# Performance work log

Hardware: AMD Instinct MI355X
Metric: run time of the kernel (lower is better)

The kernel has to match this reference:

```python
import jax, jax.numpy as jnp
import numpy as np
import math

HEAD_DIM = 64           # d_model // n_heads // 2
N_HEADS = 8
LAMBDA_INIT = 0.8 - 0.6 * math.exp(-0.3 * 6)  # depth=6
EPS = 1e-5


def setup_inputs() -> dict:
    key = jax.random.key(0)
    ks = jax.random.split(key, 8)
    B, T, S = 2, 2048, 2048
    return {
        "queries": jax.random.normal(ks[0], (B, 2 * N_HEADS, T, HEAD_DIM), jnp.float32),
        "keys": jax.random.normal(ks[1], (B, 2 * N_HEADS, S, HEAD_DIM), jnp.float32),
        "values": jax.random.normal(ks[2], (B, N_HEADS, S, 2 * HEAD_DIM), jnp.float32),
        "lambda_q1": 0.02 * jax.random.normal(ks[3], (HEAD_DIM,), jnp.float32),
        "lambda_k1": 0.02 * jax.random.normal(ks[4], (HEAD_DIM,), jnp.float32),
        "lambda_q2": 0.02 * jax.random.normal(ks[5], (HEAD_DIM,), jnp.float32),
        "lambda_k2": 0.02 * jax.random.normal(ks[6], (HEAD_DIM,), jnp.float32),
        "subln_weight": jnp.ones((2 * HEAD_DIM,), jnp.float32),
        "tgt_len": 2048,
        "src_len": 2048,
        "attn_mask": jnp.zeros((1,), jnp.bool_),
    }


def reference(queries, keys, values, lambda_q1, lambda_k1, lambda_q2, lambda_k2,
              subln_weight, tgt_len, src_len, attn_mask):
    B = queries.shape[0]
    scaling = HEAD_DIM ** -0.5
    q = queries * scaling
    # [B, 2H, T, S]
    attn_w = jnp.einsum('bhtd,bhsd->bhts', q, keys)
    attn_w = jax.nn.softmax(attn_w.astype(jnp.float32), axis=-1).astype(queries.dtype)
    lam1 = jnp.exp(jnp.sum(lambda_q1 * lambda_k1))
    lam2 = jnp.exp(jnp.sum(lambda_q2 * lambda_k2))
    lam_full = lam1 - lam2 + LAMBDA_INIT
    attn_w = attn_w.reshape(B, N_HEADS, 2, tgt_len, src_len)
    attn_w = attn_w[:, :, 0] - lam_full * attn_w[:, :, 1]   # [B, H, T, S]
    attn = jnp.einsum('bhts,bhse->bhte', attn_w, values)    # [B, H, T, 2*HEAD_DIM]
    # RMSNorm over last dim
    normed = attn * jax.lax.rsqrt(jnp.mean(jnp.square(attn.astype(jnp.float32)), axis=-1, keepdims=True) + EPS).astype(attn.dtype)
    normed = normed * subln_weight
    out = normed * (1.0 - LAMBDA_INIT)
    out = out.transpose(0, 2, 1, 3).reshape(B, tgt_len, N_HEADS * 2 * HEAD_DIM)
    return out
```

## Files before the change

### kernel.cpp

```cpp
#include <hip/hip_runtime.h>
#include <math.h>


#define NT    2048
#define D     64
#define DV    128
#define TQ    64
#define TS    32
#define NROUND (NT / (2 * TS))

#define LAMBDA_INIT 0.70082066706704814f
#define OUT_SCALE   0.29917933293295186f
#define QSCALE      0.18033688011112042f

typedef __attribute__((ext_vector_type(8)))  short    short8;
typedef __attribute__((ext_vector_type(4)))  short    short4v;
typedef __attribute__((ext_vector_type(8)))  _Float16 half8;
typedef __attribute__((ext_vector_type(2)))  __fp16   fp16x2;
typedef __attribute__((ext_vector_type(4)))  float    f32x4;
typedef unsigned short u16;
typedef unsigned int   u32;

#define MFMAH(a, b, c)  __builtin_amdgcn_mfma_f32_16x16x32_f16(a, b, c, 0, 0, 0)
#define MFMA16(a, b, c) __builtin_amdgcn_mfma_f32_16x16x32_bf16(a, b, c, 0, 0, 0)

#if __has_builtin(__builtin_amdgcn_exp2f)
#define EXP2F(x) __builtin_amdgcn_exp2f(x)
#else
#define EXP2F(x) exp2f(x)
#endif

union Hu { half8 v; _Float16 e[8]; u16 s[8]; short8 sv; };

__device__ __forceinline__ u16 f2h(float x) {
    Hu u; u.e[0] = (_Float16)x; return u.s[0];
}

__global__ __launch_bounds__(256) void prep_kv(
    const float* __restrict__ Kg, const float* __restrict__ Vg,
    const float* __restrict__ lq1, const float* __restrict__ lk1,
    const float* __restrict__ lq2, const float* __restrict__ lk2,
    u16* __restrict__ Kf, u16* __restrict__ Vf, float* __restrict__ lamw)
{
    __shared__ u16 th[64 * 136];
    const int bid = blockIdx.x;
    const int t   = threadIdx.x;
    if (bid < 2048) {
        const int idx = (bid * 256 + t) * 8;
        const float4 a = *(const float4*)(Kg + idx);
        const float4 b = *(const float4*)(Kg + idx + 4);
        Hu H;
        H.e[0] = (_Float16)a.x; H.e[1] = (_Float16)a.y;
        H.e[2] = (_Float16)a.z; H.e[3] = (_Float16)a.w;
        H.e[4] = (_Float16)b.x; H.e[5] = (_Float16)b.y;
        H.e[6] = (_Float16)b.z; H.e[7] = (_Float16)b.w;
        *(short8*)(Kf + idx) = H.sv;
        return;
    }
    if (bid == 2048) {
        if (t == 0) {
            float t1 = 0.f, t2 = 0.f;
            for (int i = 0; i < D; ++i) {
                t1 = fmaf(lq1[i], lk1[i], t1);
                t2 = fmaf(lq2[i], lk2[i], t2);
            }
            lamw[0] = __expf(t1) - __expf(t2) + LAMBDA_INIT;
        }
        return;
    }
    const int i  = bid - 2049;
    const int bh = i >> 5;
    const int eb = (i >> 4) & 1;
    const int sb = i & 15;
    const size_t vbase = (size_t)bh * NT * DV + (size_t)sb * 128 * DV + eb * 64;
    {
        const int r0 = t >> 4;
        const int c4 = (t & 15) * 4;
        #pragma unroll
        for (int rr = 0; rr < 8; ++rr) {
            const int row = r0 + rr * 16;
            const float4 x = *(const float4*)(Vg + vbase + (size_t)row * DV + c4);
            th[(c4 + 0) * 136 + row] = f2h(x.x);
            th[(c4 + 1) * 136 + row] = f2h(x.y);
            th[(c4 + 2) * 136 + row] = f2h(x.z);
            th[(c4 + 3) * 136 + row] = f2h(x.w);
        }
    }
    __syncthreads();
    const int e  = t >> 2;
    const int g  = t & 3;
    const size_t orow = ((size_t)bh * DV + eb * 64 + e) * NT + sb * 128;
    #pragma unroll
    for (int c = 0; c < 4; ++c) {
        Hu o;
        #pragma unroll
        for (int j = 0; j < 8; ++j)
            o.s[j] = th[e * 136 + g * 32 + 4 * c + (j & 3) + 16 * (j >> 2)];
        *(short8*)(Vf + orow + g * 32 + c * 8) = o.sv;
    }
}

struct SmemF {
    union {
        short8 c[4096];
        struct {
            float epi[2][32][132];
            float lbuf[2][2][2][32];
        } e;
    };
};

__global__ __launch_bounds__(512, 4) void diffattn_mfma11(
    const float* __restrict__ Qg,
    const u16* __restrict__ Kf, const u16* __restrict__ Vf,
    const float* __restrict__ lamw,
    const float* __restrict__ Wg, float* __restrict__ Outg)
{
    __shared__ SmemF sm;

    const int tid    = threadIdx.x;
    const int wv     = tid >> 6;
    const int lane   = tid & 63;
    const int quad   = lane >> 4;
    const int lc     = lane & 15;
    const int stripe = wv & 1;
    const int hh     = (wv >> 1) & 1;
    const int ks     = wv >> 2;
    const int wig    = wv & 3;
    const int qt     = blockIdx.x;
    const int bh     = blockIdx.y;
    const int b      = bh >> 3, h = bh & 7;

    const int head2b = b * 16 + 2 * h;
    const int bh8    = b * 8 + h;
    const float lam  = lamw[0];

    half8 qf[2][2];
    {
        const size_t qhead = (size_t)(head2b + hh) * NT * D;
        #pragma unroll
        for (int nq = 0; nq < 2; ++nq) {
            const int row = qt * TQ + stripe * 32 + nq * 16 + lc;
            #pragma unroll
            for (int k0 = 0; k0 < 2; ++k0) {
                const int d0 = k0 * 32 + quad * 8;
                const float4 x = *(const float4*)(Qg + qhead + (size_t)row * D + d0);
                const float4 y = *(const float4*)(Qg + qhead + (size_t)row * D + d0 + 4);
                Hu q;
                q.e[0] = (_Float16)(x.x * QSCALE); q.e[1] = (_Float16)(x.y * QSCALE);
                q.e[2] = (_Float16)(x.z * QSCALE); q.e[3] = (_Float16)(x.w * QSCALE);
                q.e[4] = (_Float16)(y.x * QSCALE); q.e[5] = (_Float16)(y.y * QSCALE);
                q.e[6] = (_Float16)(y.z * QSCALE); q.e[7] = (_Float16)(y.w * QSCALE);
                qf[nq][k0] = q.v;
            }
        }
    }

    f32x4 O_[2][8];
    #pragma unroll
    for (int nq = 0; nq < 2; ++nq)
        #pragma unroll
        for (int nt = 0; nt < 8; ++nt) O_[nq][nt] = (f32x4){0.f, 0.f, 0.f, 0.f};
    float lac[2] = {0.f, 0.f};

    u32 gK[2], gV[2];
    int kDst[2], vDst[2];
    #pragma unroll
    for (int j = 0; j < 2; ++j) {
        const int ck  = wig * 128 + lane * 2 + j;
        const int hhs = ck >> 8;
        const int n   = (ck >> 3) & 31;
        const int db  = ck & 7;
        gK[j]   = (u32)(((head2b + hhs) * NT + n) * D + db * 8);
        kDst[j] = ks * 512 + hhs * 256 + n * 8 + (db ^ (n & 7));
        const int cv = wig * 128 + lane * 2 + j;
        const int e  = cv >> 2;
        const int u  = cv & 3;
        gV[j]   = (u32)((bh8 * DV + e) * NT + u * 8);
        vDst[j] = 1024 + ks * 512 + e * 4 + (u ^ ((e >> 1) & 3));
    }

    u32 kOff[2][2];
    #pragma unroll
    for (int k0 = 0; k0 < 2; ++k0)
        #pragma unroll
        for (int mt = 0; mt < 2; ++mt)
            kOff[k0][mt] = (u32)((ks * 512 + hh * 256 + (mt * 16 + lc) * 8 +
                                  ((4 * k0 + quad) ^ (lc & 7))) * 8);
    u32 vOff[8];
    {
        const int swzv = quad ^ ((lc >> 1) & 3);
        #pragma unroll
        for (int nt = 0; nt < 8; ++nt)
            vOff[nt] = (u32)((1024 + ks * 512 + (nt * 16 + lc) * 4 + swzv) * 8);
    }

    const u16* ldsu = (const u16*)&sm.c[0];

    short8 pk[2], pv[2];
    #pragma unroll
    for (int j = 0; j < 2; ++j) {
        pk[j] = *(const short8*)(Kf + gK[j] + (u32)ks * (TS * D));
        pv[j] = *(const short8*)(Vf + gV[j] + (u32)ks * TS);
    }
    sm.c[kDst[0]] = pk[0];
    sm.c[kDst[1]] = pk[1];
    sm.c[vDst[0]] = pv[0];
    sm.c[vDst[1]] = pv[1];
    {
        const u32 tn = (u32)(2 + ks);
        #pragma unroll
        for (int j = 0; j < 2; ++j) {
            pk[j] = *(const short8*)(Kf + gK[j] + tn * (TS * D));
            pv[j] = *(const short8*)(Vf + gV[j] + tn * TS);
        }
    }
    __syncthreads();

    const fp16x2 ones = {(__fp16)1.f, (__fp16)1.f};

    for (int r = 0; r < NROUND; ++r) {
        const u32 bo = ((u32)(r & 1)) << 14;

        f32x4 sf[2][2];
        #pragma unroll
        for (int mt = 0; mt < 2; ++mt)
            #pragma unroll
            for (int nq = 0; nq < 2; ++nq) sf[mt][nq] = (f32x4){0.f, 0.f, 0.f, 0.f};
        #pragma unroll
        for (int k0 = 0; k0 < 2; ++k0) {
            #pragma unroll
            for (int mt = 0; mt < 2; ++mt) {
                const half8 kfr = *(const half8*)(ldsu + bo + kOff[k0][mt]);
                #pragma unroll
                for (int nq = 0; nq < 2; ++nq)
                    sf[mt][nq] = MFMAH(kfr, qf[nq][k0], sf[mt][nq]);
            }
        }

        if (r < NROUND - 1) {
            const int cd = ((r & 1) ^ 1) << 11;
            sm.c[cd + kDst[0]] = pk[0];
            sm.c[cd + kDst[1]] = pk[1];
            sm.c[cd + vDst[0]] = pv[0];
            sm.c[cd + vDst[1]] = pv[1];
        }
        if (r < NROUND - 2) {
            const u32 tn = (u32)(2 * (r + 2) + ks);
            #pragma unroll
            for (int j = 0; j < 2; ++j) {
                pk[j] = *(const short8*)(Kf + gK[j] + tn * (TS * D));
                pv[j] = *(const short8*)(Vf + gV[j] + tn * TS);
            }
        }

        half8 a8[2];
        #pragma unroll
        for (int nq = 0; nq < 2; ++nq) {
            union { half8 v; fp16x2 h[4]; } a;
            float ls = lac[nq];
            #pragma unroll
            for (int mt = 0; mt < 2; ++mt)
                #pragma unroll
                for (int ip = 0; ip < 2; ++ip) {
                    const float p0 = EXP2F(sf[mt][nq][2 * ip]);
                    const float p1 = EXP2F(sf[mt][nq][2 * ip + 1]);
                    const fp16x2 h2 = __builtin_amdgcn_cvt_pkrtz(p0, p1);
                    a.h[mt * 2 + ip] = h2;
                    ls = __builtin_amdgcn_fdot2(h2, ones, ls, false);
                }
            lac[nq] = ls;
            a8[nq] = a.v;
        }

        #pragma unroll
        for (int nt = 0; nt < 8; ++nt) {
            const half8 vfr = *(const half8*)(ldsu + bo + vOff[nt]);
            #pragma unroll
            for (int nq = 0; nq < 2; ++nq)
                O_[nq][nt] = MFMAH(a8[nq], vfr, O_[nq][nt]);
        }

        __syncthreads();
    }

    {
        float s0 = lac[0], s1 = lac[1];
        s0 += __shfl_xor(s0, 16); s0 += __shfl_xor(s0, 32);
        s1 += __shfl_xor(s1, 16); s1 += __shfl_xor(s1, 32);
        if (quad == 0) {
            sm.e.lbuf[hh][ks][stripe][lc]      = s0;
            sm.e.lbuf[hh][ks][stripe][16 + lc] = s1;
        }
    }
    __syncthreads();
    float coef[2][4];
    #pragma unroll
    for (int nq = 0; nq < 2; ++nq)
        #pragma unroll
        for (int i = 0; i < 4; ++i) {
            const int row = nq * 16 + quad * 4 + i;
            const float lt = sm.e.lbuf[hh][0][stripe][row] +
                             sm.e.lbuf[hh][1][stripe][row];
            coef[nq][i] = (hh == 0) ? (1.f / lt) : (-lam / lt);
        }
    __syncthreads();
    const int pid = hh * 2 + ks;
    #pragma unroll
    for (int p = 0; p < 4; ++p) {
        if (pid == p) {
            #pragma unroll
            for (int nq = 0; nq < 2; ++nq)
                #pragma unroll
                for (int i = 0; i < 4; ++i) {
                    const int row = nq * 16 + quad * 4 + i;
                    #pragma unroll
                    for (int nt = 0; nt < 8; ++nt) {
                        const int col = nt * 16 + lc;
                        const float v = O_[nq][nt][i] * coef[nq][i];
                        if (p == 0) sm.e.epi[stripe][row][col] = v;
                        else        sm.e.epi[stripe][row][col] += v;
                    }
                }
        }
        __syncthreads();
    }
    {
        const int r0 = wv * 8 + (lane >> 3);
        const int st = r0 >> 5, ri = r0 & 31;
        const int e0 = (lane & 7) * 16;
        float x[16];
        float ssq = 0.f;
        #pragma unroll
        for (int m = 0; m < 16; m += 4) {
            const float4 t4 = *(const float4*)&sm.e.epi[st][ri][e0 + m];
            x[m] = t4.x; x[m + 1] = t4.y; x[m + 2] = t4.z; x[m + 3] = t4.w;
            ssq += t4.x * t4.x + t4.y * t4.y + t4.z * t4.z + t4.w * t4.w;
        }
        ssq += __shfl_xor(ssq, 1);
        ssq += __shfl_xor(ssq, 2);
        ssq += __shfl_xor(ssq, 4);
        const float rsq = rsqrtf(ssq * (1.f / 128.f) + 1e-5f) * OUT_SCALE;
        const int rowg = qt * TQ + r0;
        const size_t base =
            ((size_t)b * NT + rowg) * (size_t)(8 * DV) + (size_t)h * DV;
        #pragma unroll
        for (int m = 0; m < 16; m += 4) {
            const float4 w4 = *(const float4*)(Wg + e0 + m);
            float4 o4;
            o4.x = x[m] * rsq * w4.x;
            o4.y = x[m + 1] * rsq * w4.y;
            o4.z = x[m + 2] * rsq * w4.z;
            o4.w = x[m + 3] * rsq * w4.w;
            *(float4*)(Outg + base + e0 + m) = o4;
        }
    }
}

__device__ __forceinline__ unsigned short f2bf(float x) {
    unsigned u = __float_as_uint(x);
    return (unsigned short)((u + 0x7fffu + ((u >> 16) & 1u)) >> 16);
}
__device__ __forceinline__ float bf2f(unsigned short h) {
    return __uint_as_float(((unsigned)h) << 16);
}

struct SmemB {
    union {
        struct {
            short8 kh[2][264];
            short8 kl[2][264];
            short8 vh[516];
            short8 vl[516];
            unsigned short ph[2][2560];
            unsigned short pl[2][2560];
        } L;
        float epi[2][32][132];
    };
};

__global__ __launch_bounds__(256, 2) void diffattn_fb(
    const float* __restrict__ Qg, const float* __restrict__ Kg,
    const float* __restrict__ Vg,
    const float* __restrict__ lq1, const float* __restrict__ lk1,
    const float* __restrict__ lq2, const float* __restrict__ lk2,
    const float* __restrict__ Wg, float* __restrict__ Outg)
{
    __shared__ SmemB sm;
    const int tid = threadIdx.x;
    const int wv = tid >> 6, lane = tid & 63;
    const int quad = lane >> 4, lc = lane & 15;
    const int stripe = wv & 1, hh = wv >> 1;
    const int qt = blockIdx.x, bh = blockIdx.y;
    const int b = bh >> 3, h = bh & 7;
    const size_t koff0 = ((size_t)(b * 16 + 2 * h)) * NT * D;
    const size_t voff  = ((size_t)(b * 8 + h)) * NT * DV;
    float t1 = 0.f, t2 = 0.f;
    for (int i = 0; i < D; ++i) {
        t1 = fmaf(lq1[i], lk1[i], t1);
        t2 = fmaf(lq2[i], lk2[i], t2);
    }
    const float lam = __expf(t1) - __expf(t2) + LAMBDA_INIT;
    short8 qfh[2][2], qfl[2][2];
    {
        const size_t qhead = ((size_t)(b * 16 + 2 * h + hh)) * NT * D;
        #pragma unroll
        for (int mt = 0; mt < 2; ++mt)
            #pragma unroll
            for (int k0 = 0; k0 < 2; ++k0) {
                const int row = qt * TQ + stripe * 32 + mt * 16 + lc;
                const int d0  = k0 * 32 + quad * 8;
                const float4 x = *(const float4*)(Qg + qhead + (size_t)row * D + d0);
                const float4 y = *(const float4*)(Qg + qhead + (size_t)row * D + d0 + 4);
                float f[8] = {x.x, x.y, x.z, x.w, y.x, y.y, y.z, y.w};
                #pragma unroll
                for (int j = 0; j < 8; ++j) {
                    const float v = f[j] * 0.125f;
                    const unsigned short hi = f2bf(v);
                    qfh[mt][k0][j] = (short)hi;
                    qfl[mt][k0][j] = (short)f2bf(v - bf2f(hi));
                }
            }
    }
    f32x4 O_[2][8];
    #pragma unroll
    for (int mt = 0; mt < 2; ++mt)
        #pragma unroll
        for (int nt = 0; nt < 8; ++nt) O_[mt][nt] = (f32x4){0.f, 0.f, 0.f, 0.f};
    float m_[2][4], l_[2][4], a_[2][4];
    #pragma unroll
    for (int mt = 0; mt < 2; ++mt)
        #pragma unroll
        for (int i = 0; i < 4; ++i) { m_[mt][i] = -1e30f; l_[mt][i] = 0.f; }
    const int s_hh = tid >> 7;
    const int s_n  = (tid >> 2) & 31;
    const int s_d0 = (tid & 3) * 16;
    const int s_e0 = tid & 31;
    const int s_s0 = ((tid >> 5) & 7) * 4;
    const int s_sb = s_s0 >> 3;
    const int s_hs = (s_s0 & 4) ? 1 : 0;
    for (int kt = 0; kt < NT / TS; ++kt) {
        const int kb = kt * TS;
        __syncthreads();
        {
            const float* kp = Kg + koff0 + (size_t)s_hh * NT * D +
                              (size_t)(kb + s_n) * D + s_d0;
            const float4 x0 = ((const float4*)kp)[0];
            const float4 x1 = ((const float4*)kp)[1];
            const float4 x2 = ((const float4*)kp)[2];
            const float4 x3 = ((const float4*)kp)[3];
            float f[16] = {x0.x, x0.y, x0.z, x0.w, x1.x, x1.y, x1.z, x1.w,
                           x2.x, x2.y, x2.z, x2.w, x3.x, x3.y, x3.z, x3.w};
            short8 c0h, c0l, c1h, c1l;
            #pragma unroll
            for (int j = 0; j < 8; ++j) {
                unsigned short hi = f2bf(f[j]);
                c0h[j] = (short)hi; c0l[j] = (short)f2bf(f[j] - bf2f(hi));
                hi = f2bf(f[8 + j]);
                c1h[j] = (short)hi; c1l[j] = (short)f2bf(f[8 + j] - bf2f(hi));
            }
            const int db0 = s_d0 >> 3;
            sm.L.kh[s_hh][db0 * 33 + s_n]       = c0h;
            sm.L.kl[s_hh][db0 * 33 + s_n]       = c0l;
            sm.L.kh[s_hh][(db0 + 1) * 33 + s_n] = c1h;
            sm.L.kl[s_hh][(db0 + 1) * 33 + s_n] = c1l;
        }
        {
            #pragma unroll
            for (int j = 0; j < 4; ++j) {
                const int e = s_e0 + 32 * j;
                float f[4];
                #pragma unroll
                for (int i = 0; i < 4; ++i)
                    f[i] = Vg[voff + (size_t)(kb + s_s0 + i) * DV + e];
                short4v hi4, lo4;
                #pragma unroll
                for (int i = 0; i < 4; ++i) {
                    const unsigned short hi = f2bf(f[i]);
                    hi4[i] = (short)hi;
                    lo4[i] = (short)f2bf(f[i] - bf2f(hi));
                }
                ((short4v*)&sm.L.vh[s_sb * 129 + e])[s_hs] = hi4;
                ((short4v*)&sm.L.vl[s_sb * 129 + e])[s_hs] = lo4;
            }
        }
        __syncthreads();
        f32x4 s_f[2][2];
        #pragma unroll
        for (int mt = 0; mt < 2; ++mt)
            #pragma unroll
            for (int nt = 0; nt < 2; ++nt) s_f[mt][nt] = (f32x4){0.f, 0.f, 0.f, 0.f};
        #pragma unroll
        for (int k0 = 0; k0 < 2; ++k0)
            #pragma unroll
            for (int nt = 0; nt < 2; ++nt) {
                const short8 kh = sm.L.kh[hh][(4 * k0 + quad) * 33 + nt * 16 + lc];
                const short8 kl = sm.L.kl[hh][(4 * k0 + quad) * 33 + nt * 16 + lc];
                #pragma unroll
                for (int mt = 0; mt < 2; ++mt) {
                    s_f[mt][nt] = MFMA16(qfh[mt][k0], kh, s_f[mt][nt]);
                    s_f[mt][nt] = MFMA16(qfl[mt][k0], kh, s_f[mt][nt]);
                    s_f[mt][nt] = MFMA16(qfh[mt][k0], kl, s_f[mt][nt]);
                }
            }
        #pragma unroll
        for (int mt = 0; mt < 2; ++mt)
            #pragma unroll
            for (int i = 0; i < 4; ++i) {
                const float v0 = s_f[mt][0][i], v1 = s_f[mt][1][i];
                float mx = fmaxf(v0, v1);
                mx = fmaxf(mx, __shfl_xor(mx, 1));
                mx = fmaxf(mx, __shfl_xor(mx, 2));
                mx = fmaxf(mx, __shfl_xor(mx, 4));
                mx = fmaxf(mx, __shfl_xor(mx, 8));
                const float mn = fmaxf(m_[mt][i], mx);
                const float al = __expf(m_[mt][i] - mn);
                const float p0 = __expf(v0 - mn);
                const float p1 = __expf(v1 - mn);
                float rs = p0 + p1;
                rs += __shfl_xor(rs, 1);
                rs += __shfl_xor(rs, 2);
                rs += __shfl_xor(rs, 4);
                rs += __shfl_xor(rs, 8);
                l_[mt][i] = l_[mt][i] * al + rs;
                m_[mt][i] = mn;
                a_[mt][i] = al;
                const int r = stripe * 32 + mt * 16 + quad * 4 + i;
                const unsigned short h0 = f2bf(p0);
                sm.L.ph[hh][r * 40 + lc]      = h0;
                sm.L.pl[hh][r * 40 + lc]      = f2bf(p0 - bf2f(h0));
                const unsigned short h1 = f2bf(p1);
                sm.L.ph[hh][r * 40 + 16 + lc] = h1;
                sm.L.pl[hh][r * 40 + 16 + lc] = f2bf(p1 - bf2f(h1));
            }
        __syncthreads();
        #pragma unroll
        for (int mt = 0; mt < 2; ++mt)
            #pragma unroll
            for (int nt = 0; nt < 8; ++nt)
                #pragma unroll
                for (int i = 0; i < 4; ++i) O_[mt][nt][i] *= a_[mt][i];
        short8 pah[2], pal[2];
        #pragma unroll
        for (int mt = 0; mt < 2; ++mt) {
            const int r = stripe * 32 + mt * 16 + lc;
            pah[mt] = *(const short8*)&sm.L.ph[hh][r * 40 + quad * 8];
            pal[mt] = *(const short8*)&sm.L.pl[hh][r * 40 + quad * 8];
        }
        #pragma unroll
        for (int nt = 0; nt < 8; ++nt) {
            const short8 vh = sm.L.vh[quad * 129 + nt * 16 + lc];
            const short8 vl = sm.L.vl[quad * 129 + nt * 16 + lc];
            #pragma unroll
            for (int mt = 0; mt < 2; ++mt) {
                O_[mt][nt] = MFMA16(pah[mt], vh, O_[mt][nt]);
                O_[mt][nt] = MFMA16(pal[mt], vh, O_[mt][nt]);
                O_[mt][nt] = MFMA16(pah[mt], vl, O_[mt][nt]);
            }
        }
    }
    __syncthreads();
    if (hh == 1) {
        #pragma unroll
        for (int mt = 0; mt < 2; ++mt)
            #pragma unroll
            for (int i = 0; i < 4; ++i) {
                const float inv = lam / l_[mt][i];
                const int r = mt * 16 + quad * 4 + i;
                #pragma unroll
                for (int nt = 0; nt < 8; ++nt)
                    sm.epi[stripe][r][nt * 16 + lc] = O_[mt][nt][i] * inv;
            }
    }
    __syncthreads();
    if (hh == 0) {
        float wvv[8];
        #pragma unroll
        for (int nt = 0; nt < 8; ++nt) wvv[nt] = Wg[nt * 16 + lc];
        #pragma unroll
        for (int mt = 0; mt < 2; ++mt)
            #pragma unroll
            for (int i = 0; i < 4; ++i) {
                const float inv1 = 1.f / l_[mt][i];
                const int r = mt * 16 + quad * 4 + i;
                float od[8];
                float ss = 0.f;
                #pragma unroll
                for (int nt = 0; nt < 8; ++nt) {
                    od[nt] = O_[mt][nt][i] * inv1 - sm.epi[stripe][r][nt * 16 + lc];
                    ss = fmaf(od[nt], od[nt], ss);
                }
                ss += __shfl_xor(ss, 1);
                ss += __shfl_xor(ss, 2);
                ss += __shfl_xor(ss, 4);
                ss += __shfl_xor(ss, 8);
                const float rsq = rsqrtf(ss * (1.f / 128.f) + 1e-5f) * OUT_SCALE;
                const int rowg = qt * TQ + stripe * 32 + r;
                const size_t base =
                    ((size_t)b * NT + rowg) * (size_t)(8 * DV) + (size_t)h * DV;
                #pragma unroll
                for (int nt = 0; nt < 8; ++nt)
                    Outg[base + nt * 16 + lc] = od[nt] * rsq * wvv[nt];
            }
    }
}

extern "C" void kernel_launch(void* const* d_in, const int* in_sizes, int n_in,
                              void* d_out, int out_size, void* d_ws, size_t ws_size,
                              hipStream_t stream) {
    const float* Q   = (const float*)d_in[0];
    const float* K   = (const float*)d_in[1];
    const float* V   = (const float*)d_in[2];
    const float* lq1 = (const float*)d_in[3];
    const float* lk1 = (const float*)d_in[4];
    const float* lq2 = (const float*)d_in[5];
    const float* lk2 = (const float*)d_in[6];
    const float* W   = (const float*)d_in[7];
    float* Out = (float*)d_out;
    const size_t NEED = 2ull * 4194304ull * sizeof(u16) + 16;
    if (ws_size >= NEED) {
        u16*   Kf   = (u16*)d_ws;
        u16*   Vf   = Kf + 4194304;
        float* lamw = (float*)(Vf + 4194304);
        prep_kv<<<2561, 256, 0, stream>>>(K, V, lq1, lk1, lq2, lk2, Kf, Vf, lamw);
        diffattn_mfma11<<<dim3(NT / TQ, 16), 512, 0, stream>>>(
            Q, Kf, Vf, lamw, W, Out);
    } else {
        diffattn_fb<<<dim3(NT / TQ, 16), 256, 0, stream>>>(
            Q, K, V, lq1, lk1, lq2, lk2, W, Out);
    }
}
```

Before: 185.5 us.

## Stream K/V tiles into LDS with direct global-to-LDS loads

Replaces the register-staged K/V prefetch (global load into registers, later ds_write into the alternate buffer) with global_load_lds DMA straight into the double-buffered LDS tiles. The swizzle moves from the LDS write side to the global source addresses, so each lane writes a contiguous 16-byte slot. Prefetch distance shrinks from two tiles to one, issued at the start of each round. This frees registers and drops the LDS store instructions, but depends on the loop's barriers and waitcnt placement to make the async LDS writes visible in time.

```diff
diff --git a/kernel.cpp b/kernel.cpp
--- a/kernel.cpp
+++ b/kernel.cpp
@@ -34,6 +34,12 @@
 
 __device__ __forceinline__ u16 f2h(float x) {
     Hu u; u.e[0] = (_Float16)x; return u.s[0];
+}
+
+__device__ __forceinline__ void glds16(const u16* g, const u16* l) {
+    __builtin_amdgcn_global_load_lds(
+        (const __attribute__((address_space(1))) void*)g,
+        (__attribute__((address_space(3))) void*)l, 16, 0, 0);
 }
 
 __global__ __launch_bounds__(256) void prep_kv(
@@ -110,7 +116,7 @@
     };
 };
 
-__global__ __launch_bounds__(512, 4) void diffattn_mfma11(
+__global__ __launch_bounds__(512, 4) void diffattn_mfma12(
     const float* __restrict__ Qg,
     const u16* __restrict__ Kf, const u16* __restrict__ Vf,
     const float* __restrict__ lamw,
@@ -163,22 +169,29 @@
         for (int nt = 0; nt < 8; ++nt) O_[nq][nt] = (f32x4){0.f, 0.f, 0.f, 0.f};
     float lac[2] = {0.f, 0.f};
 
-    u32 gK[2], gV[2];
-    int kDst[2], vDst[2];
-    #pragma unroll
-    for (int j = 0; j < 2; ++j) {
-        const int ck  = wig * 128 + lane * 2 + j;
-        const int hhs = ck >> 8;
-        const int n   = (ck >> 3) & 31;
-        const int db  = ck & 7;
-        gK[j]   = (u32)(((head2b + hhs) * NT + n) * D + db * 8);
-        kDst[j] = ks * 512 + hhs * 256 + n * 8 + (db ^ (n & 7));
-        const int cv = wig * 128 + lane * 2 + j;
-        const int e  = cv >> 2;
-        const int u  = cv & 3;
-        gV[j]   = (u32)((bh8 * DV + e) * NT + u * 8);
-        vDst[j] = 1024 + ks * 512 + e * 4 + (u ^ ((e >> 1) & 3));
-    }
+    u32 kSrc[2], vSrc[2];
+    u32 kLds[2], vLds[2];
+    #pragma unroll
+    for (int t = 0; t < 2; ++t) {
+        const int p   = (wig * 2 + t) * 64 + lane;
+        const int hhs = p >> 8;
+        const int n   = (p >> 3) & 31;
+        const int db  = (p & 7) ^ (n & 7);
+        kSrc[t] = (u32)(((head2b + hhs) * NT + n) * D + db * 8);
+        kLds[t] = (u32)((ks * 512 + (wig * 2 + t) * 64) * 16);
+        const int e = p >> 2;
+        const int u = (p & 3) ^ ((e >> 1) & 3);
+        vSrc[t] = (u32)((bh8 * DV + e) * NT + u * 8);
+        vLds[t] = (u32)((1024 + ks * 512 + (wig * 2 + t) * 64) * 16);
+    }
+    const u16* ldsu = (const u16*)&sm.c[0];
+
+    #pragma unroll
+    for (int t = 0; t < 2; ++t) {
+        glds16(Kf + kSrc[t] + (u32)ks * (TS * D), ldsu + (kLds[t] >> 1));
+        glds16(Vf + vSrc[t] + (u32)ks * TS,       ldsu + (vLds[t] >> 1));
+    }
+    __syncthreads();
 
     u32 kOff[2][2];
     #pragma unroll
@@ -195,33 +208,21 @@
             vOff[nt] = (u32)((1024 + ks * 512 + (nt * 16 + lc) * 4 + swzv) * 8);
     }
 
-    const u16* ldsu = (const u16*)&sm.c[0];
-
-    short8 pk[2], pv[2];
-    #pragma unroll
-    for (int j = 0; j < 2; ++j) {
-        pk[j] = *(const short8*)(Kf + gK[j] + (u32)ks * (TS * D));
-        pv[j] = *(const short8*)(Vf + gV[j] + (u32)ks * TS);
-    }
-    sm.c[kDst[0]] = pk[0];
-    sm.c[kDst[1]] = pk[1];
-    sm.c[vDst[0]] = pv[0];
-    sm.c[vDst[1]] = pv[1];
-    {
-        const u32 tn = (u32)(2 + ks);
-        #pragma unroll
-        for (int j = 0; j < 2; ++j) {
-            pk[j] = *(const short8*)(Kf + gK[j] + tn * (TS * D));
-            pv[j] = *(const short8*)(Vf + gV[j] + tn * TS);
-        }
-    }
-    __syncthreads();
-
     const fp16x2 ones = {(__fp16)1.f, (__fp16)1.f};
 
     for (int r = 0; r < NROUND; ++r) {
         const u32 bo = ((u32)(r & 1)) << 14;
 
+        if (r < NROUND - 1) {
+            const u32 tn = (u32)(2 * (r + 1) + ks);
+            const u32 ab = ((u32)((r + 1) & 1)) << 14;
+            #pragma unroll
+            for (int t = 0; t < 2; ++t) {
+                glds16(Kf + kSrc[t] + tn * (TS * D), ldsu + ab + (kLds[t] >> 1));
+                glds16(Vf + vSrc[t] + tn * TS,       ldsu + ab + (vLds[t] >> 1));
+            }
+        }
+
         f32x4 sf[2][2];
         #pragma unroll
         for (int mt = 0; mt < 2; ++mt)
@@ -235,22 +236,6 @@
                 #pragma unroll
                 for (int nq = 0; nq < 2; ++nq)
                     sf[mt][nq] = MFMAH(kfr, qf[nq][k0], sf[mt][nq]);
-            }
-        }
-
-        if (r < NROUND - 1) {
-            const int cd = ((r & 1) ^ 1) << 11;
-            sm.c[cd + kDst[0]] = pk[0];
-            sm.c[cd + kDst[1]] = pk[1];
-            sm.c[cd + vDst[0]] = pv[0];
-            sm.c[cd + vDst[1]] = pv[1];
-        }
-        if (r < NROUND - 2) {
-            const u32 tn = (u32)(2 * (r + 2) + ks);
-            #pragma unroll
-            for (int j = 0; j < 2; ++j) {
-                pk[j] = *(const short8*)(Kf + gK[j] + tn * (TS * D));
-                pv[j] = *(const short8*)(Vf + gV[j] + tn * TS);
             }
         }
 
@@ -623,7 +608,7 @@
         u16*   Vf   = Kf + 4194304;
         float* lamw = (float*)(Vf + 4194304);
         prep_kv<<<2561, 256, 0, stream>>>(K, V, lq1, lk1, lq2, lk2, Kf, Vf, lamw);
-        diffattn_mfma11<<<dim3(NT / TQ, 16), 512, 0, stream>>>(
+        diffattn_mfma12<<<dim3(NT / TQ, 16), 512, 0, stream>>>(
             Q, Kf, Vf, lamw, W, Out);
     } else {
         diffattn_fb<<<dim3(NT / TQ, 16), 256, 0, stream>>>(
```

New measurement: 169.6 us. 1.09x faster.
